# Performance work log

Measured on AMD Instinct MI355X. Metric: run time of the kernel, lower is better.

## Reference

```python
import jax, jax.numpy as jnp
import numpy as np

B, G, MAXITER = 8, 1024, 16
H = 1.0 / (G - 1)          # grid spacing h = (right-left)/(GridSize-1) on unit square
GD = 0.0                   # Dirichlet boundary value used by hard_encode padding

_K_CROSS = np.array([[0.0, 0.5, 0.0], [0.5, 0.0, 0.5], [0.0, 0.5, 0.0]], np.float32).reshape(1, 1, 3, 3)
_K3 = np.array([[0.0, 0.5, 0.0], [0.5, 2.0, 0.5], [0.0, 0.5, 0.0]], np.float32).reshape(1, 1, 3, 3)


def _conv3x3(x, k):
    # valid 3x3 conv, NCHW / OIHW (matches torch F.conv2d with no padding)
    return jax.lax.conv_general_dilated(x, k, (1, 1), 'VALID',
                                        dimension_numbers=('NCHW', 'OIHW', 'NCHW'))


def setup_inputs() -> dict:
    key = jax.random.key(0)
    k1, k2, k3 = jax.random.split(key, 3)
    pre = jax.random.normal(k1, (B, 1, G - 2, G - 2), dtype=jnp.float32)
    f = jax.random.normal(k2, (B, 1, G, G), dtype=jnp.float32)
    # positive coefficient field so the Jacobi divisor y3 stays bounded away from 0
    kappa = jax.random.uniform(k3, (B, 1, G, G), dtype=jnp.float32, minval=0.5, maxval=1.5)
    return {"pre": pre, "f": f, "kappa": kappa}


def reference(pre, f, kappa):
    kc = jnp.asarray(_K_CROSS, dtype=pre.dtype)
    k3 = jnp.asarray(_K3, dtype=pre.dtype)
    # loop-invariant terms: force = f_interior * h^2, w_interior, y3 = conv(w, k3)
    force = f[..., 1:-1, 1:-1] * (H * H)          # [B,1,G-2,G-2]
    w_in = kappa[..., 1:-1, 1:-1]                 # [B,1,G-2,G-2]
    y3 = _conv3x3(kappa, k3)                      # [B,1,G-2,G-2]

    def step(u, _):
        up = jnp.pad(u, ((0, 0), (0, 0), (1, 1), (1, 1)), constant_values=GD)  # hard_encode
        y1 = _conv3x3(up, kc) * w_in
        y2 = _conv3x3(kappa * up, kc)
        return (force + y1 + y2) / y3, None

    u, _ = jax.lax.scan(step, pre, None, length=MAXITER)
    return u
```

## Files before the change

kernel.cpp:

```cpp
#include <hip/hip_runtime.h>


namespace {
constexpr int    G    = 1024, Ni = 1022;
constexpr int    TOUT = 48;
constexpr size_t IMG_K = (size_t)G * G;
constexpr size_t IMG_P = (size_t)Ni * Ni;
constexpr size_t WSTR  = 1024;
constexpr size_t IMG_W = (size_t)1024 * 1024;
constexpr float  H2 = (float)(1.0 / (1023.0 * 1023.0));
}

__device__ __forceinline__ float frcp(float x) { return __builtin_amdgcn_rcpf(x); }

__device__ __forceinline__ float lane_shr1(float x) {
    return __builtin_bit_cast(float,
        __builtin_amdgcn_update_dpp(0, __builtin_bit_cast(int, x), 0x138, 0xF, 0xF, true));
}
__device__ __forceinline__ float lane_shl1(float x) {
    return __builtin_bit_cast(float,
        __builtin_amdgcn_update_dpp(0, __builtin_bit_cast(int, x), 0x130, 0xF, 0xF, true));
}

template<bool FIRST, bool LAST>
__global__ __launch_bounds__(512, 4)
void jac_fused8(const float* __restrict__ usrc, float* __restrict__ udst,
                const float* __restrict__ kap,  const float* __restrict__ fin)
{
    __shared__ __align__(16) float ex[2048];

    const int tid = threadIdx.x;
    const int w   = tid >> 6, l = tid & 63;
    const int bx = blockIdx.x, by = blockIdx.y, b = blockIdx.z;
    const int X0 = bx * TOUT - 8, Y0 = by * TOUT - 8;
    const int gx  = X0 + l;
    const int gy0 = Y0 + 8 * w;

    const float* kB = kap + (size_t)b * IMG_K;
    const float* fB = fin + (size_t)b * IMG_K;
    const bool fast = (bx >= 1) && (bx <= 20) && (by >= 1) && (by <= 20);

    float ka[10], fv[8], u[8];
    if (fast) {
        const float* kp = kB + (size_t)gy0 * G + (gx + 1);
        #pragma unroll
        for (int i = 0; i < 10; ++i) ka[i] = kp[(size_t)i * G];
        const float* fp = fB + (size_t)(gy0 + 1) * G + (gx + 1);
        #pragma unroll
        for (int r = 0; r < 8; ++r) fv[r] = fp[(size_t)r * G];
        if (FIRST) {
            const float* uS = usrc + (size_t)b * IMG_P + (size_t)gy0 * Ni + gx;
            #pragma unroll
            for (int r = 0; r < 8; ++r) u[r] = uS[(size_t)r * Ni];
        } else {
            const float* uS = usrc + (size_t)b * IMG_W + (size_t)gy0 * WSTR + gx;
            #pragma unroll
            for (int r = 0; r < 8; ++r) u[r] = uS[(size_t)r * WSTR];
        }
    } else {
        const int cx = gx + 1;
        #pragma unroll
        for (int i = 0; i < 10; ++i) {
            const int ry = gy0 + i;
            ka[i] = ((unsigned)ry < (unsigned)G && (unsigned)cx < (unsigned)G)
                  ? kB[(size_t)ry * G + cx] : 0.0f;
        }
        #pragma unroll
        for (int r = 0; r < 8; ++r) {
            const int ry = gy0 + 1 + r;
            fv[r] = ((unsigned)ry < (unsigned)G && (unsigned)cx < (unsigned)G)
                  ? fB[(size_t)ry * G + cx] : 0.0f;
        }
        if (FIRST) {
            const float* uS = usrc + (size_t)b * IMG_P;
            #pragma unroll
            for (int r = 0; r < 8; ++r) {
                const int gy = gy0 + r;
                u[r] = ((unsigned)gy < (unsigned)Ni && (unsigned)gx < (unsigned)Ni)
                     ? uS[(size_t)gy * Ni + gx] : 0.0f;
            }
        } else {
            const float* uS = usrc + (size_t)b * IMG_W;
            #pragma unroll
            for (int r = 0; r < 8; ++r) {
                const int gy = gy0 + r;
                u[r] = ((unsigned)gy < 1024u && (unsigned)gx < 1024u)
                     ? uS[(size_t)gy * WSTR + gx] : 0.0f;
            }
        }
    }

    float wN[8], wS[8], wW[8], wE[8], Fc[8];
    if (fast) {
        #pragma unroll
        for (int r = 0; r < 8; ++r) {
            const float kn = ka[r], kc = ka[r + 1], ks = ka[r + 2];
            const float kw = lane_shr1(kc), ke = lane_shl1(kc);
            const float inv = frcp(2.0f * kc + 0.5f * (kn + ks + kw + ke));
            wN[r] = 0.5f * (kc + kn) * inv;
            wS[r] = 0.5f * (kc + ks) * inv;
            wW[r] = 0.5f * (kc + kw) * inv;
            wE[r] = 0.5f * (kc + ke) * inv;
            Fc[r] = fv[r] * H2 * inv;
        }
    } else {
        #pragma unroll
        for (int r = 0; r < 8; ++r) {
            const float kn = ka[r], kc = ka[r + 1], ks = ka[r + 2];
            const float kw = lane_shr1(kc), ke = lane_shl1(kc);
            const float inv = frcp(2.0f * kc + 0.5f * (kn + ks + kw + ke));
            const int gy = gy0 + r;
            const bool dv = ((unsigned)gy < (unsigned)Ni) && ((unsigned)gx < (unsigned)Ni);
            wN[r] = dv ? 0.5f * (kc + kn) * inv : 0.0f;
            wS[r] = dv ? 0.5f * (kc + ks) * inv : 0.0f;
            wW[r] = dv ? 0.5f * (kc + kw) * inv : 0.0f;
            wE[r] = dv ? 0.5f * (kc + ke) * inv : 0.0f;
            Fc[r] = dv ? fv[r] * H2 * inv : 0.0f;
        }
    }

    const int iN = (w > 0) ? (512 + tid - 64) : (512 + tid);
    const int iS = (w < 7) ? (tid + 64)       : tid;
    #pragma unroll
    for (int t = 0; t < 8; ++t) {
        float* exb = ex + ((t & 1) << 10);
        exb[tid]       = u[0];
        exb[512 + tid] = u[7];
        __syncthreads();
        const float hN = exb[iN];
        const float hS = exb[iS];
        const float o0 = u[0], o1 = u[1], o6 = u[6], o7 = u[7];
        float prev = o0;
        #pragma unroll
        for (int r = 1; r < 7; ++r) {
            const float cur = u[r], nxt = u[r + 1];
            const float uW = lane_shr1(cur), uE = lane_shl1(cur);
            u[r] = fmaf(wN[r], prev,
                   fmaf(wS[r], nxt,
                   fmaf(wW[r], uW,
                   fmaf(wE[r], uE, Fc[r]))));
            prev = cur;
        }
        {
            const float uW = lane_shr1(o0), uE = lane_shl1(o0);
            u[0] = fmaf(wN[0], hN,
                   fmaf(wS[0], o1,
                   fmaf(wW[0], uW,
                   fmaf(wE[0], uE, Fc[0]))));
        }
        {
            const float uW = lane_shr1(o7), uE = lane_shl1(o7);
            u[7] = fmaf(wN[7], o6,
                   fmaf(wS[7], hS,
                   fmaf(wW[7], uW,
                   fmaf(wE[7], uE, Fc[7]))));
        }
    }

    if (w >= 1 && w <= 6 && l >= 8 && l < 56) {
        if (LAST) {
            float* oB = udst + (size_t)b * IMG_P;
            #pragma unroll
            for (int r = 0; r < 8; ++r) {
                const int gy = gy0 + r;
                if ((unsigned)gy < (unsigned)Ni && (unsigned)gx < (unsigned)Ni)
                    oB[(size_t)gy * Ni + gx] = u[r];
            }
        } else {
            float* oB = udst + (size_t)b * IMG_W;
            #pragma unroll
            for (int r = 0; r < 8; ++r) {
                const int gy = gy0 + r;
                if ((unsigned)gy < 1024u && (unsigned)gx < 1024u)
                    oB[(size_t)gy * WSTR + gx] = u[r];
            }
        }
    }
}

extern "C" void kernel_launch(void* const* d_in, const int* in_sizes, int n_in,
                              void* d_out, int out_size, void* d_ws, size_t ws_size,
                              hipStream_t stream)
{
    const float* pre = (const float*)d_in[0];
    const float* f   = (const float*)d_in[1];
    const float* kap = (const float*)d_in[2];
    float* out = (float*)d_out;
    float* ws  = (float*)d_ws;

    dim3 blk(512, 1, 1);
    dim3 grd((Ni + TOUT - 1) / TOUT, (Ni + TOUT - 1) / TOUT, 8);

    jac_fused8<true,  false><<<grd, blk, 0, stream>>>(pre, ws,  kap, f);
    jac_fused8<false, true ><<<grd, blk, 0, stream>>>(ws,  out, kap, f);
}
```

Baseline: 196.1 us.

## Fuse all sixteen Jacobi sweeps into one launch with 2-wide lanes and wider tiles

Replaces the two 8-sweep kernels with one kernel that runs all 16 sweeps in on-chip registers. It uses 1024-thread blocks, a 96-wide output tile with a 16-cell halo, and two columns per lane loaded as float2. This removes the intermediate workspace round trip and the second launch, and improves halo efficiency per tile. In exchange it does more redundant halo computation per block, needs more registers per thread, and splits the east/west neighbour exchange across packed pairs with DPP shifts.

```diff
diff --git a/kernel.cpp b/kernel.cpp
--- a/kernel.cpp
+++ b/kernel.cpp
@@ -3,11 +3,9 @@
 
 namespace {
 constexpr int    G    = 1024, Ni = 1022;
-constexpr int    TOUT = 48;
+constexpr int    TOUT = 96, HALO = 16;
 constexpr size_t IMG_K = (size_t)G * G;
 constexpr size_t IMG_P = (size_t)Ni * Ni;
-constexpr size_t WSTR  = 1024;
-constexpr size_t IMG_W = (size_t)1024 * 1024;
 constexpr float  H2 = (float)(1.0 / (1023.0 * 1023.0));
 }
 
@@ -22,157 +20,148 @@
         __builtin_amdgcn_update_dpp(0, __builtin_bit_cast(int, x), 0x130, 0xF, 0xF, true));
 }
 
-template<bool FIRST, bool LAST>
-__global__ __launch_bounds__(512, 4)
-void jac_fused8(const float* __restrict__ usrc, float* __restrict__ udst,
-                const float* __restrict__ kap,  const float* __restrict__ fin)
+__global__ __launch_bounds__(1024, 4)
+void jac_fused16(const float* __restrict__ pre, float* __restrict__ out,
+                 const float* __restrict__ kap, const float* __restrict__ fin)
 {
-    __shared__ __align__(16) float ex[2048];
+    __shared__ float2 ex[2][2][1024];
 
     const int tid = threadIdx.x;
-    const int w   = tid >> 6, l = tid & 63;
+    const int w = tid >> 6, l = tid & 63;
     const int bx = blockIdx.x, by = blockIdx.y, b = blockIdx.z;
-    const int X0 = bx * TOUT - 8, Y0 = by * TOUT - 8;
-    const int gx  = X0 + l;
+    const int X0 = bx * TOUT - HALO, Y0 = by * TOUT - HALO;
+    const int c0 = X0 + 2 * l;
     const int gy0 = Y0 + 8 * w;
 
     const float* kB = kap + (size_t)b * IMG_K;
     const float* fB = fin + (size_t)b * IMG_K;
-    const bool fast = (bx >= 1) && (bx <= 20) && (by >= 1) && (by <= 20);
+    const bool fast = (bx >= 1) && (bx <= 9) && (by >= 1) && (by <= 9);
 
-    float ka[10], fv[8], u[8];
+    float ko[10], kev[10];
+    float2 fv[8];
     if (fast) {
-        const float* kp = kB + (size_t)gy0 * G + (gx + 1);
+        const float* kp = kB + (size_t)gy0 * G + (c0 + 1);
         #pragma unroll
-        for (int i = 0; i < 10; ++i) ka[i] = kp[(size_t)i * G];
-        const float* fp = fB + (size_t)(gy0 + 1) * G + (gx + 1);
+        for (int i = 0; i < 10; ++i) {
+            ko[i]  = kp[(size_t)i * G];
+            kev[i] = kp[(size_t)i * G + 1];
+        }
+        const float* fp = fB + (size_t)(gy0 + 1) * G + c0;
         #pragma unroll
-        for (int r = 0; r < 8; ++r) fv[r] = fp[(size_t)r * G];
-        if (FIRST) {
-            const float* uS = usrc + (size_t)b * IMG_P + (size_t)gy0 * Ni + gx;
-            #pragma unroll
-            for (int r = 0; r < 8; ++r) u[r] = uS[(size_t)r * Ni];
-        } else {
-            const float* uS = usrc + (size_t)b * IMG_W + (size_t)gy0 * WSTR + gx;
-            #pragma unroll
-            for (int r = 0; r < 8; ++r) u[r] = uS[(size_t)r * WSTR];
-        }
+        for (int r = 0; r < 8; ++r) fv[r] = *(const float2*)(fp + (size_t)r * G);
     } else {
-        const int cx = gx + 1;
         #pragma unroll
         for (int i = 0; i < 10; ++i) {
             const int ry = gy0 + i;
-            ka[i] = ((unsigned)ry < (unsigned)G && (unsigned)cx < (unsigned)G)
-                  ? kB[(size_t)ry * G + cx] : 0.0f;
+            const bool rv = (unsigned)ry < (unsigned)G;
+            ko[i]  = (rv && (unsigned)(c0 + 1) < (unsigned)G) ? kB[(size_t)ry * G + (c0 + 1)] : 0.0f;
+            kev[i] = (rv && (unsigned)(c0 + 2) < (unsigned)G) ? kB[(size_t)ry * G + (c0 + 2)] : 0.0f;
         }
         #pragma unroll
         for (int r = 0; r < 8; ++r) {
             const int ry = gy0 + 1 + r;
-            fv[r] = ((unsigned)ry < (unsigned)G && (unsigned)cx < (unsigned)G)
-                  ? fB[(size_t)ry * G + cx] : 0.0f;
+            const bool rv = (unsigned)ry < (unsigned)G;
+            const float a = (rv && (unsigned)c0       < (unsigned)G) ? fB[(size_t)ry * G + c0]     : 0.0f;
+            const float q = (rv && (unsigned)(c0 + 1) < (unsigned)G) ? fB[(size_t)ry * G + c0 + 1] : 0.0f;
+            fv[r] = make_float2(a, q);
         }
-        if (FIRST) {
-            const float* uS = usrc + (size_t)b * IMG_P;
+    }
+
+    float2 wN[8], wS[8], wW[8], wE[8], Fc[8];
+    #pragma unroll
+    for (int r = 0; r < 8; ++r) {
+        const float kn0 = ko[r],     kn1 = kev[r];
+        const float kc0 = ko[r + 1], kc1 = kev[r + 1];
+        const float ks0 = ko[r + 2], ks1 = kev[r + 2];
+        const float kw0 = lane_shr1(kev[r + 1]);
+        const float kw1 = kc0;
+        const float ke0 = kc1;
+        const float ke1 = lane_shl1(ko[r + 1]);
+        const float inv0 = frcp(2.0f * kc0 + 0.5f * (kn0 + ks0 + kw0 + ke0));
+        const float inv1 = frcp(2.0f * kc1 + 0.5f * (kn1 + ks1 + kw1 + ke1));
+        const float fc0 = fv[r].y;
+        const float fc1 = lane_shl1(fv[r].x);
+        bool d0 = true, d1 = true;
+        if (!fast) {
+            const int gy = gy0 + r;
+            const bool rv = (unsigned)gy < (unsigned)Ni;
+            d0 = rv && (unsigned)c0       < (unsigned)Ni;
+            d1 = rv && (unsigned)(c0 + 1) < (unsigned)Ni;
+        }
+        wN[r] = make_float2(d0 ? 0.5f * (kc0 + kn0) * inv0 : 0.0f,
+                            d1 ? 0.5f * (kc1 + kn1) * inv1 : 0.0f);
+        wS[r] = make_float2(d0 ? 0.5f * (kc0 + ks0) * inv0 : 0.0f,
+                            d1 ? 0.5f * (kc1 + ks1) * inv1 : 0.0f);
+        wW[r] = make_float2(d0 ? 0.5f * (kc0 + kw0) * inv0 : 0.0f,
+                            d1 ? 0.5f * (kc1 + kw1) * inv1 : 0.0f);
+        wE[r] = make_float2(d0 ? 0.5f * (kc0 + ke0) * inv0 : 0.0f,
+                            d1 ? 0.5f * (kc1 + ke1) * inv1 : 0.0f);
+        Fc[r] = make_float2(d0 ? fc0 * H2 * inv0 : 0.0f,
+                            d1 ? fc1 * H2 * inv1 : 0.0f);
+    }
+
+    float2 u[8];
+    if (fast) {
+        const float* uS = pre + (size_t)b * IMG_P + (size_t)gy0 * Ni + c0;
+        #pragma unroll
+        for (int r = 0; r < 8; ++r) u[r] = *(const float2*)(uS + (size_t)r * Ni);
+    } else {
+        const float* uS = pre + (size_t)b * IMG_P;
+        #pragma unroll
+        for (int r = 0; r < 8; ++r) {
+            const int gy = gy0 + r;
+            const bool rv = (unsigned)gy < (unsigned)Ni;
+            const float a = (rv && (unsigned)c0       < (unsigned)Ni) ? uS[(size_t)gy * Ni + c0]     : 0.0f;
+            const float q = (rv && (unsigned)(c0 + 1) < (unsigned)Ni) ? uS[(size_t)gy * Ni + c0 + 1] : 0.0f;
+            u[r] = make_float2(a, q);
+        }
+    }
+
+    const int iN = (w > 0)  ? tid - 64 : tid;
+    const int iS = (w < 15) ? tid + 64 : tid;
+    #pragma unroll
+    for (int t = 0; t < 16; ++t) {
+        float2* top = ex[t & 1][0];
+        float2* bot = ex[t & 1][1];
+        top[tid] = u[0];
+        bot[tid] = u[7];
+        __syncthreads();
+        const float2 hN = bot[iN];
+        const float2 hS = top[iS];
+        float2 pn = hN;
+        #pragma unroll
+        for (int r = 0; r < 8; ++r) {
+            const float2 s = (r < 7) ? u[r + 1] : hS;
+            const float o0 = u[r].x, o1 = u[r].y;
+            const float uW = lane_shr1(o1);
+            const float uE = lane_shl1(o0);
+            const float v0 = fmaf(wN[r].x, pn.x,
+                             fmaf(wS[r].x, s.x,
+                             fmaf(wW[r].x, uW,
+                             fmaf(wE[r].x, o1, Fc[r].x))));
+            const float v1 = fmaf(wN[r].y, pn.y,
+                             fmaf(wS[r].y, s.y,
+                             fmaf(wW[r].y, o0,
+                             fmaf(wE[r].y, uE, Fc[r].y))));
+            pn = make_float2(o0, o1);
+            u[r] = make_float2(v0, v1);
+        }
+    }
+
+    if (w >= 2 && w < 14 && l >= 8 && l < 56) {
+        float* oB = out + (size_t)b * IMG_P;
+        if (fast) {
+            #pragma unroll
+            for (int r = 0; r < 8; ++r)
+                *(float2*)(oB + (size_t)(gy0 + r) * Ni + c0) = u[r];
+        } else {
             #pragma unroll
             for (int r = 0; r < 8; ++r) {
                 const int gy = gy0 + r;
-                u[r] = ((unsigned)gy < (unsigned)Ni && (unsigned)gx < (unsigned)Ni)
-                     ? uS[(size_t)gy * Ni + gx] : 0.0f;
-            }
-        } else {
-            const float* uS = usrc + (size_t)b * IMG_W;
-            #pragma unroll
-            for (int r = 0; r < 8; ++r) {
-                const int gy = gy0 + r;
-                u[r] = ((unsigned)gy < 1024u && (unsigned)gx < 1024u)
-                     ? uS[(size_t)gy * WSTR + gx] : 0.0f;
-            }
-        }
-    }
-
-    float wN[8], wS[8], wW[8], wE[8], Fc[8];
-    if (fast) {
-        #pragma unroll
-        for (int r = 0; r < 8; ++r) {
-            const float kn = ka[r], kc = ka[r + 1], ks = ka[r + 2];
-            const float kw = lane_shr1(kc), ke = lane_shl1(kc);
-            const float inv = frcp(2.0f * kc + 0.5f * (kn + ks + kw + ke));
-            wN[r] = 0.5f * (kc + kn) * inv;
-            wS[r] = 0.5f * (kc + ks) * inv;
-            wW[r] = 0.5f * (kc + kw) * inv;
-            wE[r] = 0.5f * (kc + ke) * inv;
-            Fc[r] = fv[r] * H2 * inv;
-        }
-    } else {
-        #pragma unroll
-        for (int r = 0; r < 8; ++r) {
-            const float kn = ka[r], kc = ka[r + 1], ks = ka[r + 2];
-            const float kw = lane_shr1(kc), ke = lane_shl1(kc);
-            const float inv = frcp(2.0f * kc + 0.5f * (kn + ks + kw + ke));
-            const int gy = gy0 + r;
-            const bool dv = ((unsigned)gy < (unsigned)Ni) && ((unsigned)gx < (unsigned)Ni);
-            wN[r] = dv ? 0.5f * (kc + kn) * inv : 0.0f;
-            wS[r] = dv ? 0.5f * (kc + ks) * inv : 0.0f;
-            wW[r] = dv ? 0.5f * (kc + kw) * inv : 0.0f;
-            wE[r] = dv ? 0.5f * (kc + ke) * inv : 0.0f;
-            Fc[r] = dv ? fv[r] * H2 * inv : 0.0f;
-        }
-    }
-
-    const int iN = (w > 0) ? (512 + tid - 64) : (512 + tid);
-    const int iS = (w < 7) ? (tid + 64)       : tid;
-    #pragma unroll
-    for (int t = 0; t < 8; ++t) {
-        float* exb = ex + ((t & 1) << 10);
-        exb[tid]       = u[0];
-        exb[512 + tid] = u[7];
-        __syncthreads();
-        const float hN = exb[iN];
-        const float hS = exb[iS];
-        const float o0 = u[0], o1 = u[1], o6 = u[6], o7 = u[7];
-        float prev = o0;
-        #pragma unroll
-        for (int r = 1; r < 7; ++r) {
-            const float cur = u[r], nxt = u[r + 1];
-            const float uW = lane_shr1(cur), uE = lane_shl1(cur);
-            u[r] = fmaf(wN[r], prev,
-                   fmaf(wS[r], nxt,
-                   fmaf(wW[r], uW,
-                   fmaf(wE[r], uE, Fc[r]))));
-            prev = cur;
-        }
-        {
-            const float uW = lane_shr1(o0), uE = lane_shl1(o0);
-            u[0] = fmaf(wN[0], hN,
-                   fmaf(wS[0], o1,
-                   fmaf(wW[0], uW,
-                   fmaf(wE[0], uE, Fc[0]))));
-        }
-        {
-            const float uW = lane_shr1(o7), uE = lane_shl1(o7);
-            u[7] = fmaf(wN[7], o6,
-                   fmaf(wS[7], hS,
-                   fmaf(wW[7], uW,
-                   fmaf(wE[7], uE, Fc[7]))));
-        }
-    }
-
-    if (w >= 1 && w <= 6 && l >= 8 && l < 56) {
-        if (LAST) {
-            float* oB = udst + (size_t)b * IMG_P;
-            #pragma unroll
-            for (int r = 0; r < 8; ++r) {
-                const int gy = gy0 + r;
-                if ((unsigned)gy < (unsigned)Ni && (unsigned)gx < (unsigned)Ni)
-                    oB[(size_t)gy * Ni + gx] = u[r];
-            }
-        } else {
-            float* oB = udst + (size_t)b * IMG_W;
-            #pragma unroll
-            for (int r = 0; r < 8; ++r) {
-                const int gy = gy0 + r;
-                if ((unsigned)gy < 1024u && (unsigned)gx < 1024u)
-                    oB[(size_t)gy * WSTR + gx] = u[r];
+                if ((unsigned)gy < (unsigned)Ni) {
+                    if ((unsigned)c0       < (unsigned)Ni) oB[(size_t)gy * Ni + c0]     = u[r].x;
+                    if ((unsigned)(c0 + 1) < (unsigned)Ni) oB[(size_t)gy * Ni + c0 + 1] = u[r].y;
+                }
             }
         }
     }
@@ -186,11 +175,10 @@
     const float* f   = (const float*)d_in[1];
     const float* kap = (const float*)d_in[2];
     float* out = (float*)d_out;
-    float* ws  = (float*)d_ws;
+    (void)d_ws; (void)ws_size;
 
-    dim3 blk(512, 1, 1);
+    dim3 blk(1024, 1, 1);
     dim3 grd((Ni + TOUT - 1) / TOUT, (Ni + TOUT - 1) / TOUT, 8);
 
-    jac_fused8<true,  false><<<grd, blk, 0, stream>>>(pre, ws,  kap, f);
-    jac_fused8<false, true ><<<grd, blk, 0, stream>>>(ws,  out, kap, f);
+    jac_fused16<<<grd, blk, 0, stream>>>(pre, out, kap, f);
 }
```

New measurement: 196.7 us. Within noise of the previous version (+0.3%).
